# Kernel tuning notes

Hardware: AMD Instinct MI355X
Metric: run time of the kernel (lower is better)

## Reference

```python
import jax, jax.numpy as jnp
import numpy as np

B, R, L = 1, 128, 256
IN_DIM, DM, DIM = 128, 32, 128  # in_dim, dim_msa, dim


def setup_inputs() -> dict:
    key = jax.random.key(0)
    k = jax.random.split(key, 6)
    x = jax.random.normal(k[0], (B, L, L, DIM), dtype=jnp.float32)
    m = jax.random.normal(k[1], (B, R, L, IN_DIM), dtype=jnp.float32)
    # proj_down1: Linear(in_dim -> dim_msa)
    W1 = jax.random.normal(k[2], (DM, IN_DIM), dtype=jnp.float32) * (1.0 / np.sqrt(IN_DIM))
    b1 = jax.random.normal(k[3], (DM,), dtype=jnp.float32) * 0.02
    # proj_down2: Linear(dim_msa**2 -> dim)
    W2 = jax.random.normal(k[4], (DIM, DM * DM), dtype=jnp.float32) * (1.0 / DM)
    b2 = jax.random.normal(k[5], (DIM,), dtype=jnp.float32) * 0.02
    return {"x": x, "m": m, "W1": W1, "b1": b1, "W2": W2, "b2": b2}


def reference(x, m, W1, b1, W2, b2):
    # proj_down1: [b, r, i, in_dim] -> [b, r, i, dim_msa]
    mp = jnp.einsum('brie,de->brid', m, W1) + b1
    nrows = mp.shape[1]
    # Original math: outer = einsum('brid,brjc->bijcd', mp, mp)/nrows,
    # then rearrange 'b i j c d -> b i j (c d)' and Linear(dm^2 -> dim).
    # Flattened index (c d) => W2[k, c*DM + d]; fuse projection into the
    # contraction so the huge [b,i,j,c,d] tensor is never materialized.
    W2r = W2.reshape(DIM, DM, DM)  # (k, c, d)
    outer = jnp.einsum('brid,brjc,kcd->bijk', mp, mp, W2r) / nrows + b2
    return x + outer
```

## Files before the change

kernel.cpp:

```cpp
#include <hip/hip_runtime.h>
#include <stdint.h>


typedef __attribute__((ext_vector_type(8))) short bf16x8;
typedef __attribute__((ext_vector_type(4))) float f32x4;

#define MFMA16 __builtin_amdgcn_mfma_f32_16x16x32_bf16

__device__ __forceinline__ unsigned short f2bf(float f) {
    union { float f; unsigned int u; } x; x.f = f;
    unsigned int r = (x.u + 0x7fffu + ((x.u >> 16) & 1u)) >> 16;
    return (unsigned short)r;
}

__device__ __forceinline__ bf16x8 load8f_bf(const float* p) {
    float4 v0 = *(const float4*)p;
    float4 v1 = *(const float4*)(p + 4);
    union { bf16x8 v; unsigned short u[8]; } r;
    r.u[0] = f2bf(v0.x); r.u[1] = f2bf(v0.y); r.u[2] = f2bf(v0.z); r.u[3] = f2bf(v0.w);
    r.u[4] = f2bf(v1.x); r.u[5] = f2bf(v1.y); r.u[6] = f2bf(v1.z); r.u[7] = f2bf(v1.w);
    return r.v;
}

__global__ __launch_bounds__(256) void prep_kernel(
    const float* __restrict__ m, const float* __restrict__ W1,
    const float* __restrict__ pb1, const float* __restrict__ W2,
    unsigned short* __restrict__ mpF, unsigned short* __restrict__ W2f)
{
    const int bx = blockIdx.x;
    if (bx >= 512) {
        const int t    = (bx - 512) * 256 + threadIdx.x;
        const int nt   = t >> 11;
        const int kc   = (t >> 6) & 31;
        const int lane = t & 63;
        const int ln   = lane & 15, q = lane >> 4;
        const float* src = W2 + (size_t)(nt * 16 + ln) * 1024 + kc;
        union { bf16x8 v; unsigned short u[8]; } r;
        #pragma unroll
        for (int j = 0; j < 8; ++j)
            r.u[j] = f2bf(src[(q * 8 + j) * 32]);
        *(bf16x8*)(W2f + (size_t)t * 8) = r.v;
        return;
    }
    const int lane = threadIdx.x & 63;
    const int w    = threadIdx.x >> 6;
    const int ln   = lane & 15, q = lane >> 4;
    const int tile = bx * 4 + w;
    const int i    = tile >> 3;
    const int r0   = (tile & 7) * 16;

    const float* Ap  = m  + ((size_t)(r0 + ln) * 256 + i) * 128 + q * 8;
    const float* Bp0 = W1 + (size_t)ln * 128 + q * 8;
    const float* Bp1 = W1 + (size_t)(16 + ln) * 128 + q * 8;

    f32x4 acc0 = {0.f, 0.f, 0.f, 0.f};
    f32x4 acc1 = {0.f, 0.f, 0.f, 0.f};
    #pragma unroll
    for (int ke = 0; ke < 4; ++ke) {
        bf16x8 a  = load8f_bf(Ap  + ke * 32);
        bf16x8 b0 = load8f_bf(Bp0 + ke * 32);
        bf16x8 b1 = load8f_bf(Bp1 + ke * 32);
        acc0 = MFMA16(a, b0, acc0, 0, 0, 0);
        acc1 = MFMA16(a, b1, acc1, 0, 0, 0);
    }
    const float bb0 = pb1[ln];
    const float bb1 = pb1[16 + ln];
    const int kr = r0 >> 5;
    const int qr = ((r0 >> 4) & 1) * 2 + (q >> 1);
    const int j0 = (q & 1) * 4;
    const size_t off0 = (size_t)(i * 2 + 0) * 2048 + kr * 512 + (qr * 16 + ln) * 8 + j0;
    const size_t off1 = (size_t)(i * 2 + 1) * 2048 + kr * 512 + (qr * 16 + ln) * 8 + j0;
    ushort4 o0, o1;
    o0.x = f2bf(acc0[0] + bb0); o0.y = f2bf(acc0[1] + bb0);
    o0.z = f2bf(acc0[2] + bb0); o0.w = f2bf(acc0[3] + bb0);
    o1.x = f2bf(acc1[0] + bb1); o1.y = f2bf(acc1[1] + bb1);
    o1.z = f2bf(acc1[2] + bb1); o1.w = f2bf(acc1[3] + bb1);
    *(ushort4*)(mpF + off0) = o0;
    *(ushort4*)(mpF + off1) = o1;
}

__device__ __forceinline__ void stage_load(const unsigned short* __restrict__ mpF,
                                           int i0, int dhalf, int tid, uint4 (&stg)[4])
{
    #pragma unroll
    for (int r = 0; r < 4; ++r) {
        const int cid = r * 512 + tid;
        const int it  = cid >> 8;
        const int pos = cid & 255;
        stg[r] = *(const uint4*)(mpF + (size_t)((i0 + it) * 2 + dhalf) * 2048 + pos * 8);
    }
}

__device__ __forceinline__ void stage_store(unsigned short* __restrict__ Bs,
                                            int tid, const uint4 (&stg)[4])
{
    #pragma unroll
    for (int r = 0; r < 4; ++r) {
        const int cid = r * 512 + tid;
        const int it  = cid >> 8;
        const int pos = cid & 255;
        *(uint4*)(Bs + it * 2048 + pos * 8) = stg[r];
    }
}

__device__ __forceinline__ void stepB(const unsigned short* __restrict__ Ab,
                                      const unsigned short* __restrict__ Bs,
                                      int wn, int lane, f32x4 (&acc)[2][4])
{
    #pragma unroll
    for (int a = 0; a < 2; ++a)
        #pragma unroll
        for (int b = 0; b < 4; ++b)
            acc[a][b] = (f32x4){0.f, 0.f, 0.f, 0.f};
    #pragma unroll
    for (int ks = 0; ks < 4; ++ks) {
        bf16x8 av[2], bv[4];
        av[0] = *(const bf16x8*)(Ab + ks * 512);
        av[1] = *(const bf16x8*)(Ab + 2048 + ks * 512);
        #pragma unroll
        for (int bn = 0; bn < 4; ++bn)
            bv[bn] = *(const bf16x8*)(Bs + (wn * 4 + bn) * 2048 + ks * 512 + lane * 8);
        #pragma unroll
        for (int am = 0; am < 2; ++am)
            #pragma unroll
            for (int bn = 0; bn < 4; ++bn)
                acc[am][bn] = MFMA16(av[am], bv[bn], acc[am][bn], 0, 0, 0);
    }
}

__device__ __forceinline__ void gwrite(unsigned short* __restrict__ Gl,
                                       const f32x4 (&acc)[2][4],
                                       int ln, int q, int wm, int wn)
{
    #pragma unroll
    for (int am = 0; am < 2; ++am) {
        const int chunk = ln * 4 + am * 2 + (q >> 1);
        const int sig   = chunk >> 3;
        const int hbase = chunk * 256 + (q & 1) * 4;
        #pragma unroll
        for (int bn = 0; bn < 4; ++bn) {
            const int p  = (wn * 4 + bn) * 4 + wm;
            const int pp = p ^ sig;
            ushort4 g;
            g.x = f2bf(acc[am][bn][0]); g.y = f2bf(acc[am][bn][1]);
            g.z = f2bf(acc[am][bn][2]); g.w = f2bf(acc[am][bn][3]);
            *(ushort4*)(Gl + hbase + pp * 8) = g;
        }
    }
}

__device__ __forceinline__ void wpre(const unsigned short* __restrict__ wp, bf16x8 (&wv)[8])
{
    #pragma unroll
    for (int k8 = 0; k8 < 8; ++k8)
        wv[k8] = *(const bf16x8*)(wp + k8 * 512);
}

__device__ __forceinline__ void stepC(const unsigned short* __restrict__ Gl,
                                      const unsigned short* __restrict__ wp,
                                      bf16x8 (&wv)[8], int ln, int q,
                                      f32x4& c0, f32x4& c1)
{
    #pragma unroll
    for (int ks = 0; ks < 16; ++ks) {
        bf16x8 cur = wv[ks & 7];
        if (ks < 8) wv[ks & 7] = *(const bf16x8*)(wp + (ks + 8) * 512);
        const int chunk = ks * 4 + q;
        const int sig   = chunk >> 3;
        const unsigned short* gp = Gl + chunk * 256 + ((ln ^ sig) << 3);
        bf16x8 ag0 = *(const bf16x8*)gp;
        bf16x8 ag1 = *(const bf16x8*)(gp + 128);
        c0 = MFMA16(ag0, cur, c0, 0, 0, 0);
        c1 = MFMA16(ag1, cur, c1, 0, 0, 0);
    }
}

__global__ __launch_bounds__(512, 4) void fused_kernel(
    const float* __restrict__ x, const float* __restrict__ b2,
    const unsigned short* __restrict__ mpF, const unsigned short* __restrict__ W2f,
    float* __restrict__ out)
{
    __shared__ __align__(16) unsigned char smem[65536];
    unsigned short* Gl = (unsigned short*)smem;
    unsigned short* Bs = (unsigned short*)(smem + 32768);

    const int tid  = threadIdx.x;
    const int lane = tid & 63, w = tid >> 6;
    const int ln   = lane & 15, q = lane >> 4;
    const int wm   = w & 3, wn = w >> 2;

    const int i0 = blockIdx.x * 8;
    const int j0 = blockIdx.y * 8;

    const unsigned short* Ab0 = mpF + (size_t)((j0 + wm) * 2) * 2048 + lane * 8;
    const unsigned short* Ab1 = Ab0 + 16384;
    const unsigned short* wp0 = W2f + (size_t)(w * 32) * 512 + lane * 8;
    const unsigned short* wp1 = wp0 + 16 * 512;

    f32x4 cacc[4];
    #pragma unroll
    for (int t = 0; t < 4; ++t) cacc[t] = (f32x4){0.f, 0.f, 0.f, 0.f};
    f32x4 acc[2][4];
    bf16x8 wv[8];
    uint4 stg[4];

    stage_load(mpF, i0, 0, tid, stg);
    stage_store(Bs, tid, stg);
    __syncthreads();

    stepB(Ab0, Bs, wn, lane, acc);
    wpre(wp0, wv);
    gwrite(Gl, acc, ln, q, wm, wn);
    __syncthreads();
    stepC(Gl, wp0, wv, ln, q, cacc[0], cacc[1]);

    stepB(Ab1, Bs, wn, lane, acc);
    __syncthreads();
    wpre(wp0, wv);
    gwrite(Gl, acc, ln, q, wm, wn);
    __syncthreads();
    stage_load(mpF, i0, 1, tid, stg);
    stepC(Gl, wp0, wv, ln, q, cacc[2], cacc[3]);
    stage_store(Bs, tid, stg);
    __syncthreads();

    stepB(Ab0, Bs, wn, lane, acc);
    wpre(wp1, wv);
    gwrite(Gl, acc, ln, q, wm, wn);
    __syncthreads();
    stepC(Gl, wp1, wv, ln, q, cacc[0], cacc[1]);

    stepB(Ab1, Bs, wn, lane, acc);
    __syncthreads();
    wpre(wp1, wv);
    gwrite(Gl, acc, ln, q, wm, wn);
    __syncthreads();

    float4 xv[4];
    size_t gb[4];
    #pragma unroll
    for (int e = 0; e < 4; ++e) {
        const int fid = e * 512 + tid;
        const int po  = fid >> 5, kq = fid & 31;
        gb[e] = ((size_t)(i0 + (po >> 3)) * 256 + (j0 + (po & 7))) * 128 + kq * 4;
        xv[e] = *(const float4*)(x + gb[e]);
    }

    stepC(Gl, wp1, wv, ln, q, cacc[2], cacc[3]);
    __syncthreads();

    float* Ep = (float*)smem;
    const float invR = 1.0f / 128.0f;
    const int kk = w * 16 + ln;
    const int u  = kk >> 2, kl = kk & 3;
    #pragma unroll
    for (int jh = 0; jh < 2; ++jh)
        #pragma unroll
        for (int pt = 0; pt < 2; ++pt)
            #pragma unroll
            for (int rg = 0; rg < 4; ++rg) {
                const int po = (pt * 4 + q) * 8 + jh * 4 + rg;
                Ep[po * 128 + ((u ^ (po & 7)) << 2) + kl] = cacc[jh * 2 + pt][rg] * invR;
            }
    __syncthreads();

    #pragma unroll
    for (int e = 0; e < 4; ++e) {
        const int fid = e * 512 + tid;
        const int po  = fid >> 5, kq = fid & 31;
        const float4 v  = *(const float4*)(Ep + po * 128 + ((kq ^ (po & 7)) << 2));
        const float4 bv = *(const float4*)(b2 + kq * 4);
        float4 o;
        o.x = xv[e].x + v.x + bv.x; o.y = xv[e].y + v.y + bv.y;
        o.z = xv[e].z + v.z + bv.z; o.w = xv[e].w + v.w + bv.w;
        *(float4*)(out + gb[e]) = o;
    }
}

extern "C" void kernel_launch(void* const* d_in, const int* in_sizes, int n_in,
                              void* d_out, int out_size, void* d_ws, size_t ws_size,
                              hipStream_t stream) {
    const float* x  = (const float*)d_in[0];
    const float* m  = (const float*)d_in[1];
    const float* W1 = (const float*)d_in[2];
    const float* b1 = (const float*)d_in[3];
    const float* W2 = (const float*)d_in[4];
    const float* b2 = (const float*)d_in[5];
    float* out = (float*)d_out;

    unsigned short* mpF = (unsigned short*)d_ws;
    unsigned short* W2f = mpF + (size_t)512 * 2048;

    prep_kernel<<<dim3(576), dim3(256), 0, stream>>>(m, W1, b1, W2, mpF, W2f);
    fused_kernel<<<dim3(32, 32), dim3(512), 0, stream>>>(x, b2, mpF, W2f, out);
}
```

Measured before the change: 141.5 us.

## Read B operand directly from global memory instead of staging in LDS

Removes the shared-memory staging buffer for the i-side mp operand, so each wave loads its B fragments straight from global/L2 memory. This halves LDS use per block to 32 KB and allows launch bounds of 8 blocks per CU instead of 4, aiming for higher occupancy and fewer barriers. Adjacent waves now load the same B data redundantly from cache, and the extra sync placement changes.

Result: slower. 271.2 us (+91.6%).

```diff
diff --git a/kernel.cpp b/kernel.cpp
--- a/kernel.cpp
+++ b/kernel.cpp
@@ -79,33 +79,9 @@
     *(ushort4*)(mpF + off1) = o1;
 }
 
-__device__ __forceinline__ void stage_load(const unsigned short* __restrict__ mpF,
-                                           int i0, int dhalf, int tid, uint4 (&stg)[4])
-{
-    #pragma unroll
-    for (int r = 0; r < 4; ++r) {
-        const int cid = r * 512 + tid;
-        const int it  = cid >> 8;
-        const int pos = cid & 255;
-        stg[r] = *(const uint4*)(mpF + (size_t)((i0 + it) * 2 + dhalf) * 2048 + pos * 8);
-    }
-}
-
-__device__ __forceinline__ void stage_store(unsigned short* __restrict__ Bs,
-                                            int tid, const uint4 (&stg)[4])
-{
-    #pragma unroll
-    for (int r = 0; r < 4; ++r) {
-        const int cid = r * 512 + tid;
-        const int it  = cid >> 8;
-        const int pos = cid & 255;
-        *(uint4*)(Bs + it * 2048 + pos * 8) = stg[r];
-    }
-}
-
 __device__ __forceinline__ void stepB(const unsigned short* __restrict__ Ab,
-                                      const unsigned short* __restrict__ Bs,
-                                      int wn, int lane, f32x4 (&acc)[2][4])
+                                      const unsigned short* __restrict__ Bb,
+                                      f32x4 (&acc)[2][4])
 {
     #pragma unroll
     for (int a = 0; a < 2; ++a)
@@ -119,7 +95,7 @@
         av[1] = *(const bf16x8*)(Ab + 2048 + ks * 512);
         #pragma unroll
         for (int bn = 0; bn < 4; ++bn)
-            bv[bn] = *(const bf16x8*)(Bs + (wn * 4 + bn) * 2048 + ks * 512 + lane * 8);
+            bv[bn] = *(const bf16x8*)(Bb + bn * 4096 + ks * 512);
         #pragma unroll
         for (int am = 0; am < 2; ++am)
             #pragma unroll
@@ -175,14 +151,13 @@
     }
 }
 
-__global__ __launch_bounds__(512, 4) void fused_kernel(
+__global__ __launch_bounds__(512, 8) void fused_kernel(
     const float* __restrict__ x, const float* __restrict__ b2,
     const unsigned short* __restrict__ mpF, const unsigned short* __restrict__ W2f,
     float* __restrict__ out)
 {
-    __shared__ __align__(16) unsigned char smem[65536];
+    __shared__ __align__(16) unsigned char smem[32768];
     unsigned short* Gl = (unsigned short*)smem;
-    unsigned short* Bs = (unsigned short*)(smem + 32768);
 
     const int tid  = threadIdx.x;
     const int lane = tid & 63, w = tid >> 6;
@@ -194,6 +169,7 @@
 
     const unsigned short* Ab0 = mpF + (size_t)((j0 + wm) * 2) * 2048 + lane * 8;
     const unsigned short* Ab1 = Ab0 + 16384;
+    const unsigned short* Bb  = mpF + (size_t)((i0 + wn * 4) * 2) * 2048 + lane * 8;
     const unsigned short* wp0 = W2f + (size_t)(w * 32) * 512 + lane * 8;
     const unsigned short* wp1 = wp0 + 16 * 512;
 
@@ -202,35 +178,28 @@
     for (int t = 0; t < 4; ++t) cacc[t] = (f32x4){0.f, 0.f, 0.f, 0.f};
     f32x4 acc[2][4];
     bf16x8 wv[8];
-    uint4 stg[4];
-
-    stage_load(mpF, i0, 0, tid, stg);
-    stage_store(Bs, tid, stg);
-    __syncthreads();
-
-    stepB(Ab0, Bs, wn, lane, acc);
+
+    stepB(Ab0, Bb, acc);
     wpre(wp0, wv);
     gwrite(Gl, acc, ln, q, wm, wn);
     __syncthreads();
     stepC(Gl, wp0, wv, ln, q, cacc[0], cacc[1]);
 
-    stepB(Ab1, Bs, wn, lane, acc);
+    stepB(Ab1, Bb, acc);
     __syncthreads();
     wpre(wp0, wv);
     gwrite(Gl, acc, ln, q, wm, wn);
     __syncthreads();
-    stage_load(mpF, i0, 1, tid, stg);
     stepC(Gl, wp0, wv, ln, q, cacc[2], cacc[3]);
-    stage_store(Bs, tid, stg);
-    __syncthreads();
-
-    stepB(Ab0, Bs, wn, lane, acc);
+
+    stepB(Ab0, Bb + 2048, acc);
+    __syncthreads();
     wpre(wp1, wv);
     gwrite(Gl, acc, ln, q, wm, wn);
     __syncthreads();
     stepC(Gl, wp1, wv, ln, q, cacc[0], cacc[1]);
 
-    stepB(Ab1, Bs, wn, lane, acc);
+    stepB(Ab1, Bb + 2048, acc);
     __syncthreads();
     wpre(wp1, wv);
     gwrite(Gl, acc, ln, q, wm, wn);
```
